# Kernel optimization log

Measured on AMD Instinct MI355X. Metric: run time of the kernel, lower is better.

Reference implementation:

```python
import jax, jax.numpy as jnp
import numpy as np

B, T, F, E = 256, 256, 8, 128
H = 2 * E  # hidden_dim = 2*embedding_dim = 256
NL = 5     # num_layers per LSTM stack


def setup_inputs() -> dict:
    key = jax.random.key(0)
    ks = jax.random.split(key, 9)
    s1 = 1.0 / np.sqrt(H)
    s2 = 1.0 / np.sqrt(E)
    u = lambda k, shape, s: jax.random.uniform(k, shape, jnp.float32, -s, s)
    return {
        "x": jax.random.normal(ks[0], (B, T, F), jnp.float32),
        # stack 1: input F -> hidden H, 5 layers. b = b_ih + b_hh combined.
        "w_ih0_1": u(ks[1], (4 * H, F), s1),
        "w_ihr_1": u(ks[2], (NL - 1, 4 * H, H), s1),
        "w_hh_1": u(ks[3], (NL, 4 * H, H), s1),
        "b_1": u(ks[4], (NL, 4 * H), s1),
        # stack 2: input H -> hidden E, 5 layers
        "w_ih0_2": u(ks[5], (4 * E, H), s2),
        "w_ihr_2": u(ks[6], (NL - 1, 4 * E, E), s2),
        "w_hh_2": u(ks[7], (NL, 4 * E, E), s2),
        "b_2": u(ks[8], (NL, 4 * E), s2),
    }


def _lstm_layer(x, w_ih, w_hh, b):
    """x: [B,T,D] -> (outputs [B,T,Hd], final hidden [B,Hd]). PyTorch gate order i,f,g,o."""
    Hd = w_hh.shape[-1]
    # precompute input contribution for all timesteps (the big GEMM)
    xg = jnp.einsum('btd,gd->tbg', x, w_ih) + b  # [T,B,4Hd]
    h0 = jnp.zeros((x.shape[0], Hd), x.dtype)

    def step(carry, xt):
        h, c = carry
        g = xt + h @ w_hh.T
        i, f, gg, o = jnp.split(g, 4, axis=-1)
        c = jax.nn.sigmoid(f) * c + jax.nn.sigmoid(i) * jnp.tanh(gg)
        h = jax.nn.sigmoid(o) * jnp.tanh(c)
        return (h, c), h

    (h, _), hs = jax.lax.scan(step, (h0, h0), xg)
    return jnp.swapaxes(hs, 0, 1), h


def _stack(x, w_ih0, w_ihr, w_hh, b):
    y, h = _lstm_layer(x, w_ih0, w_hh[0], b[0])
    for l in range(1, w_hh.shape[0]):
        y, h = _lstm_layer(y, w_ihr[l - 1], w_hh[l], b[l])
    return y, h


def reference(x, w_ih0_1, w_ihr_1, w_hh_1, b_1, w_ih0_2, w_ihr_2, w_hh_2, b_2):
    x = x.reshape(x.shape[0], T, F)
    y, _ = _stack(x, w_ih0_1, w_ihr_1, w_hh_1, b_1)   # [B,T,H]
    _, h = _stack(y, w_ih0_2, w_ihr_2, w_hh_2, b_2)   # h: [B,E] last layer final hidden
    return h
```

## Files before the change

### kernel.cpp

```cpp
#include <hip/hip_runtime.h>
#include <math.h>

typedef unsigned short u16;
typedef unsigned int   u32;
typedef unsigned long long u64;
typedef __bf16 bf16x8 __attribute__((ext_vector_type(8)));
typedef float  f32x4  __attribute__((ext_vector_type(4)));

#define BB 256
#define TT 256
#define HD 256
#define ED 128
#define NSTEPS 265

#define H_U32   (10 * 2 * BB * HD)
#define CTR_OFF H_U32
#define CTR_U32 256
#define XP_OFF  (H_U32 + CTR_U32)
#define XP_U32  (BB * TT * 8)
#define WT_OFF  (XP_OFF + XP_U32)

__constant__ size_t g_woff[10] = {0ul,589824ul,1638400ul,2686976ul,3735552ul,
                                  4784128ul,5177344ul,5439488ul,5701632ul,5963776ul};
__constant__ int g_cb[11] = {0,73728,204800,335872,466944,598016,
                             647168,679936,712704,745472,778240};

__device__ __forceinline__ u16 f2bf_hi(float f) {
    u32 u = __float_as_uint(f);
    u32 r = (u + 0x7FFFu + ((u >> 16) & 1u)) >> 16;
    return (u16)r;
}
__device__ __forceinline__ float bf2f(u16 h) { return __uint_as_float(((u32)h) << 16); }
__device__ __forceinline__ float sigmoidf_(float v) { return 1.0f / (1.0f + expf(-v)); }

__global__ __launch_bounds__(256) void zero_state(u32* wsd) {
    const int n = XP_OFF;
    for (int i = blockIdx.x * blockDim.x + threadIdx.x; i < n; i += gridDim.x * blockDim.x)
        wsd[i] = 0u;
}

__global__ __launch_bounds__(256) void conv_x(const float* __restrict__ x, u32* __restrict__ wsd) {
    u32* xp = wsd + XP_OFF;
    for (int i = blockIdx.x * blockDim.x + threadIdx.x; i < XP_U32; i += gridDim.x * blockDim.x) {
        float v = x[i];
        u16 hi = f2bf_hi(v);
        u16 lo = f2bf_hi(v - bf2f(hi));
        xp[i] = (u32)hi | ((u32)lo << 16);
    }
}

__global__ __launch_bounds__(256) void conv_all(
    const float* __restrict__ w_ih0_1, const float* __restrict__ w_ihr_1,
    const float* __restrict__ w_hh_1,
    const float* __restrict__ w_ih0_2, const float* __restrict__ w_ihr_2,
    const float* __restrict__ w_hh_2,
    u32* __restrict__ wsd)
{
    __bf16* dst0 = (__bf16*)(wsd + WT_OFF);
    const int nch = 778240;
    for (int ci = blockIdx.x * blockDim.x + threadIdx.x; ci < nch;
         ci += gridDim.x * blockDim.x) {
        int l = 0;
        while (ci >= g_cb[l + 1]) ++l;
        int di = ci - g_cb[l];

        const int hd  = (l < 5) ? 256 : 128;
        const int din = (l == 0) ? 32 : ((l < 6) ? 256 : 128);
        const int xw  = (l == 0) ? 8 : din;
        const int Kp  = din + hd;
        const int nk  = Kp >> 5;

        const float *wih, *whh; int wihld, whhld;
        if (l == 0)      { wih = w_ih0_1;                                whh = w_hh_1;
                           wihld = 8;   whhld = 256; }
        else if (l < 5)  { wih = w_ihr_1 + (size_t)(l - 1) * 1024 * 256; whh = w_hh_1 + (size_t)l * 1024 * 256;
                           wihld = 256; whhld = 256; }
        else if (l == 5) { wih = w_ih0_2;                                whh = w_hh_2;
                           wihld = 256; whhld = 128; }
        else             { wih = w_ihr_2 + (size_t)(l - 6) * 512 * 128;  whh = w_hh_2 + (size_t)(l - 5) * 512 * 128;
                           wihld = 128; whhld = 128; }

        int lane = di & 63;
        int rem  = di >> 6;
        int kt   = rem % nk;
        int rem2 = rem / nk;
        int p    = rem2 & 1;
        int g    = (rem2 >> 1) & 3;
        int jt   = rem2 >> 3;
        int r15  = lane & 15, kq = lane >> 4;
        int row  = g * hd + jt * 16 + r15;

        bf16x8 o8;
        #pragma unroll
        for (int e = 0; e < 8; ++e) {
            int k = kt * 32 + kq * 8 + e;
            float v = 0.0f;
            if (k < xw) v = wih[(size_t)row * wihld + k];
            else if (k >= din && k < Kp) v = whh[(size_t)row * whhld + (k - din)];
            __bf16 h = (__bf16)v;
            o8[e] = p ? (__bf16)(v - (float)h) : h;
        }
        *(bf16x8*)(dst0 + g_woff[l] + (size_t)di * 8) = o8;
    }
}

__device__ __forceinline__ void unpack8(const uint4& a, const uint4& b, bf16x8& bh, bf16x8& bl) {
    union { u32 u[4]; bf16x8 v; } H, L;
    H.u[0] = (a.x & 0xFFFFu) | (a.y << 16);
    H.u[1] = (a.z & 0xFFFFu) | (a.w << 16);
    H.u[2] = (b.x & 0xFFFFu) | (b.y << 16);
    H.u[3] = (b.z & 0xFFFFu) | (b.w << 16);
    L.u[0] = (a.x >> 16) | (a.y & 0xFFFF0000u);
    L.u[1] = (a.z >> 16) | (a.w & 0xFFFF0000u);
    L.u[2] = (b.x >> 16) | (b.y & 0xFFFF0000u);
    L.u[3] = (b.z >> 16) | (b.w & 0xFFFF0000u);
    bh = H.v; bl = L.v;
}

__global__ __launch_bounds__(512, 2) void lstm_persist(
    const float* __restrict__ b_1, const float* __restrict__ b_2,
    u32* __restrict__ wsd, float* __restrict__ out)
{
    __shared__ __align__(16) u16 A_sh[65536];

    const int bid = blockIdx.x;
    const int xcd = bid & 7, slot = bid >> 3;
    int l, jt, bt;
    if (xcd < 5)      { l = xcd;               bt = slot >> 4;        jt = slot & 15; }
    else if (xcd == 5){ l = 5 + (slot >> 4);   bt = (slot >> 3) & 1;  jt = slot & 7; }
    else if (xcd == 6){ l = 7 + (slot >> 4);   bt = (slot >> 3) & 1;  jt = slot & 7; }
    else              { if (slot >= 16) return; l = 9; bt = slot >> 3; jt = slot & 7; }

    const int hd  = (l < 5) ? 256 : 128;
    const int din = (l == 0) ? 32 : ((l < 6) ? 256 : 128);
    const int nk  = (din + hd) >> 5;
    const float* bias = (l < 5) ? (b_1 + l * 1024) : (b_2 + (l - 5) * 512);

    u32* hbuf = wsd;
    u32* ctr  = wsd + CTR_OFF;
    const u32* xp = wsd + XP_OFF;
    const u16* wt = (const u16*)(wsd + WT_OFF);

    const int tid  = threadIdx.x;
    const int lane = tid & 63;
    const int wv   = tid >> 6;
    const int r15  = lane & 15;
    const int kq   = lane >> 4;
    const int brow = bt * 128 + wv * 16 + r15;
    const int j0   = jt * 16 + kq * 4;

    {
        const uint4* src = (const uint4*)(wt + g_woff[l] + (size_t)jt * 8 * nk * 512);
        uint4* dst = (uint4*)A_sh;
        const int n4 = nk * 512;
        for (int i = tid; i < n4; i += 512) dst[i] = src[i];
    }
    __syncthreads();

    float bgr[4][4];
    #pragma unroll
    for (int g = 0; g < 4; ++g) {
        float4 v = *(const float4*)&bias[g * hd + j0];
        bgr[g][0] = v.x; bgr[g][1] = v.y; bgr[g][2] = v.z; bgr[g][3] = v.w;
    }

    int offH[4], offL[4];
    #pragma unroll
    for (int g = 0; g < 4; ++g) {
        offH[g] = (g * 2)     * nk * 512 + lane * 8;
        offL[g] = (g * 2 + 1) * nk * 512 + lane * 8;
    }

    float4 cv = make_float4(0.f, 0.f, 0.f, 0.f);
    const int lm = (l > 0) ? (l - 1) : 0;

    for (int w = 0; w < NSTEPS; ++w) {
        const int t = w - l;
        if (t >= 0 && t < TT) {
            const u32* hin   = hbuf + ((size_t)lm * 2 + (t & 1)) * (BB * HD);
            const u32* hprev = hbuf + ((size_t)l * 2 + ((t & 1) ^ 1)) * (BB * HD);
            u32*       hout  = hbuf + ((size_t)l * 2 + (t & 1)) * (BB * HD);

            auto loadB = [&](int kt, uint4& A, uint4& B) {
                if (l == 0) {
                    if (kt == 0) {
                        if (kq == 0) {
                            const uint4* p = (const uint4*)(xp + ((size_t)brow * TT + t) * 8);
                            A = p[0]; B = p[1];
                        } else { A = make_uint4(0,0,0,0); B = make_uint4(0,0,0,0); }
                    } else {
                        const u32* p = hprev + (size_t)brow * HD + (kt * 32 - 32) + kq * 8;
                        A = *(const uint4*)p; B = *(const uint4*)(p + 4);
                    }
                } else {
                    int k0 = kt * 32 + kq * 8;
                    const u32* p = (k0 < din) ? (hin + (size_t)brow * HD + k0)
                                              : (hprev + (size_t)brow * HD + (k0 - din));
                    A = *(const uint4*)p; B = *(const uint4*)(p + 4);
                }
            };

            f32x4 acc0 = {0.f,0.f,0.f,0.f}, acc1 = {0.f,0.f,0.f,0.f};
            f32x4 acc2 = {0.f,0.f,0.f,0.f}, acc3 = {0.f,0.f,0.f,0.f};

            uint4 cA, cB, nA, nB;
            loadB(0, cA, cB);
            if (nk > 1) loadB(1, nA, nB);

            for (int kt = 0; kt < nk; ++kt) {
                uint4 fA, fB;
                if (kt + 2 < nk) loadB(kt + 2, fA, fB);

                bf16x8 bh, bl;
                unpack8(cA, cB, bh, bl);

                const int kof = kt * 512;
                bf16x8 a0h = *(const bf16x8*)&A_sh[offH[0] + kof];
                bf16x8 a1h = *(const bf16x8*)&A_sh[offH[1] + kof];
                bf16x8 a2h = *(const bf16x8*)&A_sh[offH[2] + kof];
                bf16x8 a3h = *(const bf16x8*)&A_sh[offH[3] + kof];
                bf16x8 a0l = *(const bf16x8*)&A_sh[offL[0] + kof];
                bf16x8 a1l = *(const bf16x8*)&A_sh[offL[1] + kof];
                bf16x8 a2l = *(const bf16x8*)&A_sh[offL[2] + kof];
                bf16x8 a3l = *(const bf16x8*)&A_sh[offL[3] + kof];

                acc0 = __builtin_amdgcn_mfma_f32_16x16x32_bf16(a0h, bh, acc0, 0, 0, 0);
                acc1 = __builtin_amdgcn_mfma_f32_16x16x32_bf16(a1h, bh, acc1, 0, 0, 0);
                acc2 = __builtin_amdgcn_mfma_f32_16x16x32_bf16(a2h, bh, acc2, 0, 0, 0);
                acc3 = __builtin_amdgcn_mfma_f32_16x16x32_bf16(a3h, bh, acc3, 0, 0, 0);
                acc0 = __builtin_amdgcn_mfma_f32_16x16x32_bf16(a0h, bl, acc0, 0, 0, 0);
                acc1 = __builtin_amdgcn_mfma_f32_16x16x32_bf16(a1h, bl, acc1, 0, 0, 0);
                acc2 = __builtin_amdgcn_mfma_f32_16x16x32_bf16(a2h, bl, acc2, 0, 0, 0);
                acc3 = __builtin_amdgcn_mfma_f32_16x16x32_bf16(a3h, bl, acc3, 0, 0, 0);
                acc0 = __builtin_amdgcn_mfma_f32_16x16x32_bf16(a0l, bh, acc0, 0, 0, 0);
                acc1 = __builtin_amdgcn_mfma_f32_16x16x32_bf16(a1l, bh, acc1, 0, 0, 0);
                acc2 = __builtin_amdgcn_mfma_f32_16x16x32_bf16(a2l, bh, acc2, 0, 0, 0);
                acc3 = __builtin_amdgcn_mfma_f32_16x16x32_bf16(a3l, bh, acc3, 0, 0, 0);

                cA = nA; cB = nB; nA = fA; nB = fB;
            }

            float4 hv;
            {
                float i_, f_, g_, o_;
                i_ = sigmoidf_(acc0[0] + bgr[0][0]); f_ = sigmoidf_(acc1[0] + bgr[1][0]);
                g_ = tanhf   (acc2[0] + bgr[2][0]); o_ = sigmoidf_(acc3[0] + bgr[3][0]);
                cv.x = fmaf(f_, cv.x, i_ * g_); hv.x = o_ * tanhf(cv.x);
                i_ = sigmoidf_(acc0[1] + bgr[0][1]); f_ = sigmoidf_(acc1[1] + bgr[1][1]);
                g_ = tanhf   (acc2[1] + bgr[2][1]); o_ = sigmoidf_(acc3[1] + bgr[3][1]);
                cv.y = fmaf(f_, cv.y, i_ * g_); hv.y = o_ * tanhf(cv.y);
                i_ = sigmoidf_(acc0[2] + bgr[0][2]); f_ = sigmoidf_(acc1[2] + bgr[1][2]);
                g_ = tanhf   (acc2[2] + bgr[2][2]); o_ = sigmoidf_(acc3[2] + bgr[3][2]);
                cv.z = fmaf(f_, cv.z, i_ * g_); hv.z = o_ * tanhf(cv.z);
                i_ = sigmoidf_(acc0[3] + bgr[0][3]); f_ = sigmoidf_(acc1[3] + bgr[1][3]);
                g_ = tanhf   (acc2[3] + bgr[2][3]); o_ = sigmoidf_(acc3[3] + bgr[3][3]);
                cv.w = fmaf(f_, cv.w, i_ * g_); hv.w = o_ * tanhf(cv.w);
            }

            u32 pk0, pk1, pk2, pk3;
            {
                u16 h0 = f2bf_hi(hv.x); pk0 = (u32)h0 | ((u32)f2bf_hi(hv.x - bf2f(h0)) << 16);
                u16 h1 = f2bf_hi(hv.y); pk1 = (u32)h1 | ((u32)f2bf_hi(hv.y - bf2f(h1)) << 16);
                u16 h2 = f2bf_hi(hv.z); pk2 = (u32)h2 | ((u32)f2bf_hi(hv.z - bf2f(h2)) << 16);
                u16 h3 = f2bf_hi(hv.w); pk3 = (u32)h3 | ((u32)f2bf_hi(hv.w - bf2f(h3)) << 16);
            }
            u64* hp = (u64*)(hout + (size_t)brow * HD + j0);
            __hip_atomic_store(hp + 0, (u64)pk0 | ((u64)pk1 << 32), __ATOMIC_RELAXED, __HIP_MEMORY_SCOPE_AGENT);
            __hip_atomic_store(hp + 1, (u64)pk2 | ((u64)pk3 << 32), __ATOMIC_RELAXED, __HIP_MEMORY_SCOPE_AGENT);

            if (l == 9 && t == TT - 1)
                *(float4*)&out[(size_t)brow * ED + j0] = hv;
        }

        __syncthreads();
        if (tid == 0) {
            __hip_atomic_fetch_add(&ctr[xcd * 32], 1u,
                                   __ATOMIC_RELAXED, __HIP_MEMORY_SCOPE_AGENT);
            const u32 w1 = (u32)(w + 1);
            for (int it = 0; it < (1 << 22); ++it) {
                bool ok = true;
                #pragma unroll
                for (int r = 0; r < 8; ++r) {
                    u32 tgt = ((r == 7) ? 16u : 32u) * w1;
                    ok &= (__hip_atomic_load(&ctr[r * 32], __ATOMIC_RELAXED,
                                             __HIP_MEMORY_SCOPE_AGENT) >= tgt);
                }
                if (ok) break;
                __builtin_amdgcn_s_sleep(2);
            }
            __builtin_amdgcn_fence(__ATOMIC_ACQUIRE, "agent");
        }
        __syncthreads();
    }
}

extern "C" void kernel_launch(void* const* d_in, const int* in_sizes, int n_in,
                              void* d_out, int out_size, void* d_ws, size_t ws_size,
                              hipStream_t stream) {
    const float* x       = (const float*)d_in[0];
    const float* w_ih0_1 = (const float*)d_in[1];
    const float* w_ihr_1 = (const float*)d_in[2];
    const float* w_hh_1  = (const float*)d_in[3];
    const float* b_1     = (const float*)d_in[4];
    const float* w_ih0_2 = (const float*)d_in[5];
    const float* w_ihr_2 = (const float*)d_in[6];
    const float* w_hh_2  = (const float*)d_in[7];
    const float* b_2     = (const float*)d_in[8];
    u32*   wsd = (u32*)d_ws;
    float* out = (float*)d_out;

    hipLaunchKernelGGL(zero_state, dim3(1024), dim3(256), 0, stream, wsd);
    hipLaunchKernelGGL(conv_all, dim3(1024), dim3(256), 0, stream,
                       w_ih0_1, w_ihr_1, w_hh_1, w_ih0_2, w_ihr_2, w_hh_2, wsd);
    hipLaunchKernelGGL(conv_x, dim3(256), dim3(256), 0, stream, x, wsd);
    hipLaunchKernelGGL(lstm_persist, dim3(256), dim3(512), 0, stream,
                       b_1, b_2, wsd, out);
}
```

Baseline: 3.374 ms.

## Template per-layer K loop with deep prefetch and use a single-master grid barrier

The persistent LSTM kernel body becomes a template specialised per layer shape. This fully unrolls the K loop and keeps up to 8 B-operand tiles in flight in registers, replacing the previous 2-deep rolling prefetch. The grid barrier is also changed: only block 0 polls the eight per-XCD counters and then publishes a release word, while every other block spins on that one word with a shorter sleep. The aim is to hide global-load latency and reduce atomic polling traffic, at the cost of higher register pressure and an extra hop of latency through the master block.

```diff
diff --git a/kernel.cpp b/kernel.cpp
--- a/kernel.cpp
+++ b/kernel.cpp
@@ -15,7 +15,7 @@
 
 #define H_U32   (10 * 2 * BB * HD)
 #define CTR_OFF H_U32
-#define CTR_U32 256
+#define CTR_U32 512
 #define XP_OFF  (H_U32 + CTR_U32)
 #define XP_U32  (BB * TT * 8)
 #define WT_OFF  (XP_OFF + XP_U32)
@@ -117,29 +117,13 @@
     bh = H.v; bl = L.v;
 }
 
-__global__ __launch_bounds__(512, 2) void lstm_persist(
-    const float* __restrict__ b_1, const float* __restrict__ b_2,
-    u32* __restrict__ wsd, float* __restrict__ out)
+template<int NKI, int NKT, bool ISL0>
+__device__ void run_persist(int l, int bid, int xcd, int jt, int bt, int hd,
+    const float* __restrict__ bias, u32* __restrict__ hbuf, u32* __restrict__ ctr,
+    const u32* __restrict__ xp, float* __restrict__ out, const u16* __restrict__ A_sh)
 {
-    __shared__ __align__(16) u16 A_sh[65536];
-
-    const int bid = blockIdx.x;
-    const int xcd = bid & 7, slot = bid >> 3;
-    int l, jt, bt;
-    if (xcd < 5)      { l = xcd;               bt = slot >> 4;        jt = slot & 15; }
-    else if (xcd == 5){ l = 5 + (slot >> 4);   bt = (slot >> 3) & 1;  jt = slot & 7; }
-    else if (xcd == 6){ l = 7 + (slot >> 4);   bt = (slot >> 3) & 1;  jt = slot & 7; }
-    else              { if (slot >= 16) return; l = 9; bt = slot >> 3; jt = slot & 7; }
-
-    const int hd  = (l < 5) ? 256 : 128;
-    const int din = (l == 0) ? 32 : ((l < 6) ? 256 : 128);
-    const int nk  = (din + hd) >> 5;
-    const float* bias = (l < 5) ? (b_1 + l * 1024) : (b_2 + (l - 5) * 512);
-
-    u32* hbuf = wsd;
-    u32* ctr  = wsd + CTR_OFF;
-    const u32* xp = wsd + XP_OFF;
-    const u16* wt = (const u16*)(wsd + WT_OFF);
+    constexpr int DIN = NKI * 32;
+    constexpr int RD  = (NKT < 8) ? NKT : 8;
 
     const int tid  = threadIdx.x;
     const int lane = tid & 63;
@@ -149,14 +133,6 @@
     const int brow = bt * 128 + wv * 16 + r15;
     const int j0   = jt * 16 + kq * 4;
 
-    {
-        const uint4* src = (const uint4*)(wt + g_woff[l] + (size_t)jt * 8 * nk * 512);
-        uint4* dst = (uint4*)A_sh;
-        const int n4 = nk * 512;
-        for (int i = tid; i < n4; i += 512) dst[i] = src[i];
-    }
-    __syncthreads();
-
     float bgr[4][4];
     #pragma unroll
     for (int g = 0; g < 4; ++g) {
@@ -167,8 +143,8 @@
     int offH[4], offL[4];
     #pragma unroll
     for (int g = 0; g < 4; ++g) {
-        offH[g] = (g * 2)     * nk * 512 + lane * 8;
-        offL[g] = (g * 2 + 1) * nk * 512 + lane * 8;
+        offH[g] = (g * 2)     * NKT * 512 + lane * 8;
+        offL[g] = (g * 2 + 1) * NKT * 512 + lane * 8;
     }
 
     float4 cv = make_float4(0.f, 0.f, 0.f, 0.f);
@@ -181,8 +157,8 @@
             const u32* hprev = hbuf + ((size_t)l * 2 + ((t & 1) ^ 1)) * (BB * HD);
             u32*       hout  = hbuf + ((size_t)l * 2 + (t & 1)) * (BB * HD);
 
-            auto loadB = [&](int kt, uint4& A, uint4& B) {
-                if (l == 0) {
+            auto ldB = [&](int kt, uint4& A, uint4& B) {
+                if constexpr (ISL0) {
                     if (kt == 0) {
                         if (kq == 0) {
                             const uint4* p = (const uint4*)(xp + ((size_t)brow * TT + t) * 8);
@@ -193,9 +169,9 @@
                         A = *(const uint4*)p; B = *(const uint4*)(p + 4);
                     }
                 } else {
-                    int k0 = kt * 32 + kq * 8;
-                    const u32* p = (k0 < din) ? (hin + (size_t)brow * HD + k0)
-                                              : (hprev + (size_t)brow * HD + (k0 - din));
+                    const int k0 = kt * 32 + kq * 8;
+                    const u32* p = (kt < NKI) ? (hin + (size_t)brow * HD + k0)
+                                              : (hprev + (size_t)brow * HD + (k0 - DIN));
                     A = *(const uint4*)p; B = *(const uint4*)(p + 4);
                 }
             };
@@ -203,16 +179,15 @@
             f32x4 acc0 = {0.f,0.f,0.f,0.f}, acc1 = {0.f,0.f,0.f,0.f};
             f32x4 acc2 = {0.f,0.f,0.f,0.f}, acc3 = {0.f,0.f,0.f,0.f};
 
-            uint4 cA, cB, nA, nB;
-            loadB(0, cA, cB);
-            if (nk > 1) loadB(1, nA, nB);
-
-            for (int kt = 0; kt < nk; ++kt) {
-                uint4 fA, fB;
-                if (kt + 2 < nk) loadB(kt + 2, fA, fB);
-
+            uint4 rA[RD], rB[RD];
+            #pragma unroll
+            for (int i = 0; i < RD; ++i) ldB(i, rA[i], rB[i]);
+
+            #pragma unroll
+            for (int kt = 0; kt < NKT; ++kt) {
                 bf16x8 bh, bl;
-                unpack8(cA, cB, bh, bl);
+                unpack8(rA[kt % RD], rB[kt % RD], bh, bl);
+                if (kt + RD < NKT) ldB(kt + RD, rA[kt % RD], rB[kt % RD]);
 
                 const int kof = kt * 512;
                 bf16x8 a0h = *(const bf16x8*)&A_sh[offH[0] + kof];
@@ -236,8 +211,6 @@
                 acc1 = __builtin_amdgcn_mfma_f32_16x16x32_bf16(a1l, bh, acc1, 0, 0, 0);
                 acc2 = __builtin_amdgcn_mfma_f32_16x16x32_bf16(a2l, bh, acc2, 0, 0, 0);
                 acc3 = __builtin_amdgcn_mfma_f32_16x16x32_bf16(a3l, bh, acc3, 0, 0, 0);
-
-                cA = nA; cB = nB; nA = fA; nB = fB;
             }
 
             float4 hv;
@@ -277,21 +250,72 @@
             __hip_atomic_fetch_add(&ctr[xcd * 32], 1u,
                                    __ATOMIC_RELAXED, __HIP_MEMORY_SCOPE_AGENT);
             const u32 w1 = (u32)(w + 1);
-            for (int it = 0; it < (1 << 22); ++it) {
-                bool ok = true;
-                #pragma unroll
-                for (int r = 0; r < 8; ++r) {
-                    u32 tgt = ((r == 7) ? 16u : 32u) * w1;
-                    ok &= (__hip_atomic_load(&ctr[r * 32], __ATOMIC_RELAXED,
-                                             __HIP_MEMORY_SCOPE_AGENT) >= tgt);
+            if (bid == 0) {
+                for (int it = 0; it < (1 << 22); ++it) {
+                    bool ok = true;
+                    #pragma unroll
+                    for (int r = 0; r < 8; ++r) {
+                        u32 tgt = ((r == 7) ? 16u : 32u) * w1;
+                        ok &= (__hip_atomic_load(&ctr[r * 32], __ATOMIC_RELAXED,
+                                                 __HIP_MEMORY_SCOPE_AGENT) >= tgt);
+                    }
+                    if (ok) break;
+                    __builtin_amdgcn_s_sleep(1);
                 }
-                if (ok) break;
-                __builtin_amdgcn_s_sleep(2);
+                __hip_atomic_store(&ctr[256], w1, __ATOMIC_RELAXED, __HIP_MEMORY_SCOPE_AGENT);
+            } else {
+                for (int it = 0; it < (1 << 22); ++it) {
+                    if (__hip_atomic_load(&ctr[256], __ATOMIC_RELAXED,
+                                          __HIP_MEMORY_SCOPE_AGENT) >= w1) break;
+                    __builtin_amdgcn_s_sleep(1);
+                }
             }
             __builtin_amdgcn_fence(__ATOMIC_ACQUIRE, "agent");
         }
         __syncthreads();
     }
+}
+
+__global__ __launch_bounds__(512, 2) void lstm_persist(
+    const float* __restrict__ b_1, const float* __restrict__ b_2,
+    u32* __restrict__ wsd, float* __restrict__ out)
+{
+    __shared__ __align__(16) u16 A_sh[65536];
+
+    const int bid = blockIdx.x;
+    const int xcd = bid & 7, slot = bid >> 3;
+    int l, jt, bt;
+    if (xcd < 5)      { l = xcd;               bt = slot >> 4;        jt = slot & 15; }
+    else if (xcd == 5){ l = 5 + (slot >> 4);   bt = (slot >> 3) & 1;  jt = slot & 7; }
+    else if (xcd == 6){ l = 7 + (slot >> 4);   bt = (slot >> 3) & 1;  jt = slot & 7; }
+    else              { if (slot >= 16) return; l = 9; bt = slot >> 3; jt = slot & 7; }
+
+    const int hd  = (l < 5) ? 256 : 128;
+    const int din = (l == 0) ? 32 : ((l < 6) ? 256 : 128);
+    const int nk  = (din + hd) >> 5;
+    const float* bias = (l < 5) ? (b_1 + l * 1024) : (b_2 + (l - 5) * 512);
+
+    u32* hbuf = wsd;
+    u32* ctr  = wsd + CTR_OFF;
+    const u32* xp = wsd + XP_OFF;
+    const u16* wt = (const u16*)(wsd + WT_OFF);
+
+    {
+        const uint4* src = (const uint4*)(wt + g_woff[l] + (size_t)jt * 8 * nk * 512);
+        uint4* dst = (uint4*)A_sh;
+        const int n4 = nk * 512;
+        for (int i = threadIdx.x; i < n4; i += 512) dst[i] = src[i];
+    }
+    __syncthreads();
+
+    if (l == 0)
+        run_persist<1, 9, true >(l, bid, xcd, jt, bt, hd, bias, hbuf, ctr, xp, out, A_sh);
+    else if (l < 5)
+        run_persist<8, 16, false>(l, bid, xcd, jt, bt, hd, bias, hbuf, ctr, xp, out, A_sh);
+    else if (l == 5)
+        run_persist<8, 12, false>(l, bid, xcd, jt, bt, hd, bias, hbuf, ctr, xp, out, A_sh);
+    else
+        run_persist<4, 8, false>(l, bid, xcd, jt, bt, hd, bias, hbuf, ctr, xp, out, A_sh);
 }
 
 extern "C" void kernel_launch(void* const* d_in, const int* in_sizes, int n_in,
```

After: 3.286 ms. 2.6% less time.
